# Performance work log

Hardware: AMD Instinct MI355X
Metric: run time of the kernel (lower is better)

Reference implementation:

```python
import jax, jax.numpy as jnp
import numpy as np

N_NODES = 50000
N_EDGES = 800000
N_FEAT = 128
HIDDEN = 256
N_GRAPHS = 256
N_CLASSES = 10
BN_EPS = 1e-5


def setup_inputs() -> dict:
    key = jax.random.key(0)
    ks = jax.random.split(key, 12)
    s = 1.0 / np.sqrt(HIDDEN)
    inp = {
        "x": jax.random.normal(ks[0], (N_NODES, N_FEAT), dtype=jnp.float32),
        "edge_index": jax.random.randint(ks[1], (2, N_EDGES), 0, N_NODES, dtype=jnp.int64),
        "batch": jnp.sort(jax.random.randint(ks[2], (N_NODES,), 0, N_GRAPHS, dtype=jnp.int64)),
        "conv1_w0": jax.random.normal(ks[3], (N_FEAT, HIDDEN), dtype=jnp.float32) / np.sqrt(N_FEAT),
        "conv1_b0": jnp.zeros((HIDDEN,), jnp.float32),
        "conv1_w1": jax.random.normal(ks[4], (HIDDEN, HIDDEN), dtype=jnp.float32) * s,
        "conv1_b1": jnp.zeros((HIDDEN,), jnp.float32),
        "conv1_bn_gamma": jnp.ones((HIDDEN,), jnp.float32),
        "conv1_bn_beta": jnp.zeros((HIDDEN,), jnp.float32),
        "conv1_bn_mean": jnp.zeros((HIDDEN,), jnp.float32),
        "conv1_bn_var": jnp.ones((HIDDEN,), jnp.float32),
        "convs_w0": jax.random.normal(ks[5], (3, HIDDEN, HIDDEN), dtype=jnp.float32) * s,
        "convs_b0": jnp.zeros((3, HIDDEN), jnp.float32),
        "convs_w1": jax.random.normal(ks[6], (3, HIDDEN, HIDDEN), dtype=jnp.float32) * s,
        "convs_b1": jnp.zeros((3, HIDDEN), jnp.float32),
        "convs_bn_gamma": jnp.ones((3, HIDDEN), jnp.float32),
        "convs_bn_beta": jnp.zeros((3, HIDDEN), jnp.float32),
        "convs_bn_mean": jnp.zeros((3, HIDDEN), jnp.float32),
        "convs_bn_var": jnp.ones((3, HIDDEN), jnp.float32),
        "eps": jnp.zeros((4,), jnp.float32),
        "lin1_w": jax.random.normal(ks[7], (HIDDEN, HIDDEN), dtype=jnp.float32) * s,
        "lin1_b": jnp.zeros((HIDDEN,), jnp.float32),
        "lin2_w": jax.random.normal(ks[8], (HIDDEN, N_CLASSES), dtype=jnp.float32) * s,
        "lin2_b": jnp.zeros((N_CLASSES,), jnp.float32),
    }
    return inp


def _gin_conv(x, src, dst, eps, w0, b0, w1, b1, g, be, m, v):
    # message = x[src]; aggregate = scatter_add at dst; update = MLP((1+eps)*x + aggr)
    aggr = jax.ops.segment_sum(x[src], dst, num_segments=N_NODES)
    h = (1.0 + eps) * x + aggr
    h = jax.nn.relu(h @ w0 + b0)
    h = jax.nn.relu(h @ w1 + b1)
    return (h - m) * jax.lax.rsqrt(v + BN_EPS) * g + be  # eval-mode BatchNorm1d


def reference(x, edge_index, batch,
              conv1_w0, conv1_b0, conv1_w1, conv1_b1,
              conv1_bn_gamma, conv1_bn_beta, conv1_bn_mean, conv1_bn_var,
              convs_w0, convs_b0, convs_w1, convs_b1,
              convs_bn_gamma, convs_bn_beta, convs_bn_mean, convs_bn_var,
              eps, lin1_w, lin1_b, lin2_w, lin2_b):
    src, dst = edge_index[0], edge_index[1]
    h = _gin_conv(x, src, dst, eps[0], conv1_w0, conv1_b0, conv1_w1, conv1_b1,
                  conv1_bn_gamma, conv1_bn_beta, conv1_bn_mean, conv1_bn_var)
    for i in range(convs_w0.shape[0]):
        h = _gin_conv(h, src, dst, eps[i + 1], convs_w0[i], convs_b0[i],
                      convs_w1[i], convs_b1[i], convs_bn_gamma[i], convs_bn_beta[i],
                      convs_bn_mean[i], convs_bn_var[i])
    # global_mean_pool over graph ids
    sums = jax.ops.segment_sum(h, batch, num_segments=N_GRAPHS)
    cnts = jax.ops.segment_sum(jnp.ones((N_NODES,), h.dtype), batch, num_segments=N_GRAPHS)
    pooled = sums / jnp.maximum(cnts, 1.0)[:, None]
    h = jax.nn.relu(pooled @ lin1_w + lin1_b)  # dropout is identity at inference
    logits = h @ lin2_w + lin2_b
    return jax.nn.log_softmax(logits, axis=-1)
```

## Files before the change

### kernel.cpp

```cpp
#include <hip/hip_runtime.h>
#include <hip/hip_bf16.h>

#define N_NODES 50000
#define N_EDGES 800000
#define N_FEAT 128
#define HIDDEN 256
#define N_GRAPHS 256
#define N_CLASSES 10
#define SCAN_NB ((N_NODES + 255) / 256)

typedef __hip_bfloat16 bf16_t;
typedef short bf16x8 __attribute__((ext_vector_type(8)));
typedef float f32x4 __attribute__((ext_vector_type(4)));

__device__ inline float bfb2f(short s) {
    unsigned u = ((unsigned)(unsigned short)s) << 16;
    float f; __builtin_memcpy(&f, &u, 4); return f;
}
__device__ inline short f2bfb(float f) {
    bf16_t b = __float2bfloat16(f);
    short s; __builtin_memcpy(&s, &b, 2); return s;
}


__global__ void count_deg_kernel(const int* __restrict__ ei, unsigned* __restrict__ deg) {
    int e = blockIdx.x * blockDim.x + threadIdx.x;
    if (e < N_EDGES) atomicAdd(&deg[ei[N_EDGES + e]], 1u);
}

__global__ __launch_bounds__(256) void scan_a_kernel(const unsigned* __restrict__ deg,
                                                     unsigned* __restrict__ rowptr,
                                                     unsigned* __restrict__ blocksum) {
    __shared__ unsigned tmp[256];
    int t = threadIdx.x;
    int g = blockIdx.x * 256 + t;
    unsigned v = (g < N_NODES) ? deg[g] : 0u;
    tmp[t] = v;
    __syncthreads();
    #pragma unroll
    for (int off = 1; off < 256; off <<= 1) {
        unsigned add = (t >= off) ? tmp[t - off] : 0u;
        __syncthreads();
        tmp[t] += add;
        __syncthreads();
    }
    if (g < N_NODES) rowptr[g] = tmp[t] - v;
    if (t == 255) blocksum[blockIdx.x] = tmp[t];
}

__global__ __launch_bounds__(256) void scan_b_kernel(unsigned* __restrict__ blocksum) {
    __shared__ unsigned tmp[256];
    int t = threadIdx.x;
    unsigned v = (t < SCAN_NB) ? blocksum[t] : 0u;
    tmp[t] = v;
    __syncthreads();
    #pragma unroll
    for (int off = 1; off < 256; off <<= 1) {
        unsigned add = (t >= off) ? tmp[t - off] : 0u;
        __syncthreads();
        tmp[t] += add;
        __syncthreads();
    }
    if (t < SCAN_NB) blocksum[t] = tmp[t] - v;
}

__global__ __launch_bounds__(256) void scan_c_kernel(unsigned* __restrict__ rowptr,
                                                     const unsigned* __restrict__ blocksum,
                                                     unsigned* __restrict__ cursor) {
    int g = blockIdx.x * 256 + threadIdx.x;
    if (g < N_NODES) {
        unsigned r = rowptr[g] + blocksum[blockIdx.x];
        rowptr[g] = r;
        cursor[g] = r;
    }
    if (g == 0) rowptr[N_NODES] = N_EDGES;
}

__global__ void fill_adj_kernel(const int* __restrict__ ei, unsigned* __restrict__ cursor,
                                int* __restrict__ adj) {
    int e = blockIdx.x * blockDim.x + threadIdx.x;
    if (e < N_EDGES) {
        int src = ei[e];
        int dst = ei[N_EDGES + e];
        unsigned pos = atomicAdd(&cursor[dst], 1u);
        adj[pos] = src;
    }
}


__global__ __launch_bounds__(256) void convert_x_kernel(const float* __restrict__ x,
                                                        bf16_t* __restrict__ xb) {
    int i = blockIdx.x * 256 + threadIdx.x;
    if (i < N_NODES * N_FEAT / 4) {
        float4 v = reinterpret_cast<const float4*>(x)[i];
        short4 o;
        o.x = f2bfb(v.x); o.y = f2bfb(v.y); o.z = f2bfb(v.z); o.w = f2bfb(v.w);
        reinterpret_cast<short4*>(xb)[i] = o;
    }
}


__global__ __launch_bounds__(256) void prep_weights_kernel(
    const float* __restrict__ c1_w0, const float* __restrict__ c1_w1,
    const float* __restrict__ cs_w0, const float* __restrict__ cs_w1,
    bf16_t* __restrict__ wt)
{
    __shared__ float T[32][33];
    int z = blockIdx.z;
    const float* src; int K; size_t off;
    if (z == 0)      { src = c1_w0; K = N_FEAT;  off = 0; }
    else if (z == 1) { src = c1_w1; K = HIDDEN;  off = 32768; }
    else {
        int i = (z - 2) >> 1;
        src = (((z - 2) & 1) ? cs_w1 : cs_w0) + (size_t)i * HIDDEN * HIDDEN;
        K = HIDDEN;
        off = 32768 + (size_t)(z - 1) * 65536;
    }
    int k0 = blockIdx.x * 32, n0 = blockIdx.y * 32;
    if (k0 >= K) return;
    int t = threadIdx.x;
    int r = t >> 3, c4 = (t & 7) * 4;
    float4 v = *reinterpret_cast<const float4*>(src + (size_t)(k0 + r) * HIDDEN + n0 + c4);
    T[r][c4 + 0] = v.x; T[r][c4 + 1] = v.y; T[r][c4 + 2] = v.z; T[r][c4 + 3] = v.w;
    __syncthreads();
    int n = t >> 3, kc = (t & 7) * 4;
    short4 o;
    o.x = f2bfb(T[kc + 0][n]); o.y = f2bfb(T[kc + 1][n]);
    o.z = f2bfb(T[kc + 2][n]); o.w = f2bfb(T[kc + 3][n]);
    *reinterpret_cast<short4*>((short*)wt + off + (size_t)(n0 + n) * K + k0 + kc) = o;
}


__global__ __launch_bounds__(256) void aggregate1_kernel(
    const bf16_t* __restrict__ xb, const int* __restrict__ adj,
    const unsigned* __restrict__ rowptr, const float* __restrict__ eps_arr,
    bf16_t* __restrict__ out)
{
    int w = threadIdx.x >> 6, lane = threadIdx.x & 63;
    int n = blockIdx.x * 4 + w;
    if (n >= N_NODES) return;
    int q = lane >> 4, l4 = lane & 15;
    unsigned beg = rowptr[n], end = rowptr[n + 1];
    const short* xs = (const short*)xb;
    float acc[8] = {};
    unsigned e = beg;
    for (; e + 8 <= end; e += 8) {
        int s0 = adj[e + q];
        int s1 = adj[e + 4 + q];
        bf16x8 v0 = *reinterpret_cast<const bf16x8*>(xs + (unsigned)s0 * N_FEAT + l4 * 8);
        bf16x8 v1 = *reinterpret_cast<const bf16x8*>(xs + (unsigned)s1 * N_FEAT + l4 * 8);
        #pragma unroll
        for (int j = 0; j < 8; j++) acc[j] += bfb2f(v0[j]) + bfb2f(v1[j]);
    }
    for (; e + 4 <= end; e += 4) {
        int s0 = adj[e + q];
        bf16x8 v0 = *reinterpret_cast<const bf16x8*>(xs + (unsigned)s0 * N_FEAT + l4 * 8);
        #pragma unroll
        for (int j = 0; j < 8; j++) acc[j] += bfb2f(v0[j]);
    }
    int rem = (int)(end - e);
    if (q < rem) {
        bf16x8 v0 = *reinterpret_cast<const bf16x8*>(xs + (unsigned)adj[e + q] * N_FEAT + l4 * 8);
        #pragma unroll
        for (int j = 0; j < 8; j++) acc[j] += bfb2f(v0[j]);
    }
    if (q == 0) {
        bf16x8 sv = *reinterpret_cast<const bf16x8*>(xs + (unsigned)n * N_FEAT + l4 * 8);
        float ep = 1.f + eps_arr[0];
        #pragma unroll
        for (int j = 0; j < 8; j++) acc[j] += ep * bfb2f(sv[j]);
    }
    #pragma unroll
    for (int j = 0; j < 8; j++) {
        acc[j] += __shfl_xor(acc[j], 16);
        acc[j] += __shfl_xor(acc[j], 32);
    }
    if (lane < 16) {
        bf16x8 o;
        #pragma unroll
        for (int j = 0; j < 8; j++) o[j] = f2bfb(acc[j]);
        *reinterpret_cast<bf16x8*>((short*)out + (unsigned)n * N_FEAT + l4 * 8) = o;
    }
}


__global__ __launch_bounds__(256) void aggregate2_kernel(
    const bf16_t* __restrict__ x, const int* __restrict__ adj,
    const unsigned* __restrict__ rowptr, const float* __restrict__ eps_arr, int eps_idx,
    bf16_t* __restrict__ out)
{
    int w = threadIdx.x >> 6, lane = threadIdx.x & 63;
    int n = blockIdx.x * 4 + w;
    if (n >= N_NODES) return;
    int half = lane >> 5, l5 = lane & 31;
    unsigned beg = rowptr[n], end = rowptr[n + 1];
    const short* xs = (const short*)x;
    float acc[8] = {};
    unsigned e = beg;
    for (; e + 8 <= end; e += 8) {
        int s0 = adj[e + half];
        int s1 = adj[e + 2 + half];
        int s2 = adj[e + 4 + half];
        int s3 = adj[e + 6 + half];
        bf16x8 v0 = *reinterpret_cast<const bf16x8*>(xs + (unsigned)s0 * HIDDEN + l5 * 8);
        bf16x8 v1 = *reinterpret_cast<const bf16x8*>(xs + (unsigned)s1 * HIDDEN + l5 * 8);
        bf16x8 v2 = *reinterpret_cast<const bf16x8*>(xs + (unsigned)s2 * HIDDEN + l5 * 8);
        bf16x8 v3 = *reinterpret_cast<const bf16x8*>(xs + (unsigned)s3 * HIDDEN + l5 * 8);
        #pragma unroll
        for (int j = 0; j < 8; j++)
            acc[j] += (bfb2f(v0[j]) + bfb2f(v1[j])) + (bfb2f(v2[j]) + bfb2f(v3[j]));
    }
    for (; e + 2 <= end; e += 2) {
        int s0 = adj[e + half];
        bf16x8 v0 = *reinterpret_cast<const bf16x8*>(xs + (unsigned)s0 * HIDDEN + l5 * 8);
        #pragma unroll
        for (int j = 0; j < 8; j++) acc[j] += bfb2f(v0[j]);
    }
    if (e < end && half == 0) {
        bf16x8 v0 = *reinterpret_cast<const bf16x8*>(xs + (unsigned)adj[e] * HIDDEN + l5 * 8);
        #pragma unroll
        for (int j = 0; j < 8; j++) acc[j] += bfb2f(v0[j]);
    }
    if (half == 0) {
        bf16x8 sv = *reinterpret_cast<const bf16x8*>(xs + (unsigned)n * HIDDEN + l5 * 8);
        float ep = 1.f + eps_arr[eps_idx];
        #pragma unroll
        for (int j = 0; j < 8; j++) acc[j] += ep * bfb2f(sv[j]);
    }
    #pragma unroll
    for (int j = 0; j < 8; j++) acc[j] += __shfl_xor(acc[j], 32);
    if (half == 0) {
        bf16x8 o;
        #pragma unroll
        for (int j = 0; j < 8; j++) o[j] = f2bfb(acc[j]);
        *reinterpret_cast<bf16x8*>((short*)out + (unsigned)n * HIDDEN + l5 * 8) = o;
    }
}


#define GBM 128
#define GBN 128
#define GBK 64

__global__ __launch_bounds__(512) void gemm_bf16_kernel(
    const bf16_t* __restrict__ A, const bf16_t* __restrict__ Wt,
    const float* __restrict__ bias, bf16_t* __restrict__ C,
    int M, int K,
    const float* __restrict__ bn_g, const float* __restrict__ bn_b,
    const float* __restrict__ bn_m, const float* __restrict__ bn_v, int do_bn)
{
    __shared__ short lds[18432];
    short (*As)[72] = reinterpret_cast<short(*)[72]>(lds);
    short (*Bs)[72] = reinterpret_cast<short(*)[72]>(lds + 9216);
    short (*Cs)[136] = reinterpret_cast<short(*)[136]>(lds);

    int tid = threadIdx.x;
    int lane = tid & 63;
    int wave = tid >> 6;
    int wr = wave >> 2, wc = wave & 3;
    int row0 = blockIdx.x * GBM, col0 = blockIdx.y * GBN;

    int lrow = tid >> 3, lch = tid & 7;

    const short* Ab = (const short*)A;
    const short* Wb = (const short*)Wt;

    f32x4 acc[4][2] = {};

    for (int k0 = 0; k0 < K; k0 += GBK) {
        #pragma unroll
        for (int rr = 0; rr < 2; rr++) {
            int r = lrow + rr * 64;
            int arow = row0 + r;
            bf16x8 av = {};
            if (arow < M)
                av = *reinterpret_cast<const bf16x8*>(Ab + (size_t)arow * K + k0 + lch * 8);
            *reinterpret_cast<bf16x8*>(&As[r][lch * 8]) = av;
            bf16x8 bv = *reinterpret_cast<const bf16x8*>(Wb + (size_t)(col0 + r) * K + k0 + lch * 8);
            *reinterpret_cast<bf16x8*>(&Bs[r][lch * 8]) = bv;
        }
        __syncthreads();

        int fr = lane & 15, fk = (lane >> 4) * 8;
        #pragma unroll
        for (int ks = 0; ks < 2; ks++) {
            bf16x8 a[4], b[2];
            #pragma unroll
            for (int m = 0; m < 4; m++)
                a[m] = *reinterpret_cast<const bf16x8*>(&As[wr * 64 + m * 16 + fr][ks * 32 + fk]);
            #pragma unroll
            for (int n = 0; n < 2; n++)
                b[n] = *reinterpret_cast<const bf16x8*>(&Bs[wc * 32 + n * 16 + fr][ks * 32 + fk]);
            #pragma unroll
            for (int m = 0; m < 4; m++)
                #pragma unroll
                for (int n = 0; n < 2; n++)
                    acc[m][n] = __builtin_amdgcn_mfma_f32_16x16x32_bf16(a[m], b[n], acc[m][n], 0, 0, 0);
        }
        __syncthreads();
    }

    #pragma unroll
    for (int m = 0; m < 4; m++) {
        #pragma unroll
        for (int n = 0; n < 2; n++) {
            int rl = wr * 64 + m * 16 + (lane >> 4) * 4;
            int cl = wc * 32 + n * 16 + (lane & 15);
            int c = col0 + cl;
            float bi = bias[c];
            #pragma unroll
            for (int r = 0; r < 4; r++) {
                float v = acc[m][n][r] + bi;
                v = fmaxf(v, 0.f);
                if (do_bn) v = (v - bn_m[c]) * rsqrtf(bn_v[c] + 1e-5f) * bn_g[c] + bn_b[c];
                Cs[rl + r][cl] = f2bfb(v);
            }
        }
    }
    __syncthreads();
    int lr = tid >> 2, c16 = tid & 3;
    int r = row0 + lr;
    if (r < M) {
        short* Cb = (short*)C;
        #pragma unroll
        for (int cc = 0; cc < 4; cc++) {
            int ch = c16 + cc * 4;
            bf16x8 cv = *reinterpret_cast<const bf16x8*>(&Cs[lr][ch * 8]);
            *reinterpret_cast<bf16x8*>(Cb + (size_t)r * HIDDEN + col0 + ch * 8) = cv;
        }
    }
}


__global__ __launch_bounds__(256) void pool_kernel(const bf16_t* __restrict__ h,
                                                   const int* __restrict__ batch,
                                                   float* __restrict__ pooled) {
    __shared__ int sbs[2];
    __shared__ float red[4][HIDDEN];
    int g = blockIdx.x;
    if (threadIdx.x == 0) {
        int lo = 0, hi = N_NODES;
        while (lo < hi) { int mid = (lo + hi) >> 1; if (batch[mid] < g) lo = mid + 1; else hi = mid; }
        sbs[0] = lo;
        hi = N_NODES;
        while (lo < hi) { int mid = (lo + hi) >> 1; if (batch[mid] < g + 1) lo = mid + 1; else hi = mid; }
        sbs[1] = lo;
    }
    __syncthreads();
    int sbeg = sbs[0], send = sbs[1];
    int w = threadIdx.x >> 6, lane = threadIdx.x & 63;
    int half = lane >> 5, l5 = lane & 31;
    const short* hb = (const short*)h;
    float acc[8] = {};
    for (int n = sbeg + w * 2 + half; n < send; n += 8) {
        bf16x8 v = *reinterpret_cast<const bf16x8*>(hb + (size_t)n * HIDDEN + l5 * 8);
        #pragma unroll
        for (int j = 0; j < 8; j++) acc[j] += bfb2f(v[j]);
    }
    #pragma unroll
    for (int j = 0; j < 8; j++) acc[j] += __shfl_xor(acc[j], 32);
    if (half == 0) {
        #pragma unroll
        for (int j = 0; j < 8; j++) red[w][l5 * 8 + j] = acc[j];
    }
    __syncthreads();
    int t = threadIdx.x;
    float s = red[0][t] + red[1][t] + red[2][t] + red[3][t];
    float cnt = (float)(send - sbeg);
    pooled[g * HIDDEN + t] = s / fmaxf(cnt, 1.f);
}


__global__ void head_kernel(const float* __restrict__ pooled,
                            const float* __restrict__ w1, const float* __restrict__ b1,
                            const float* __restrict__ w2, const float* __restrict__ b2,
                            float* __restrict__ out) {
    int g = blockIdx.x, t = threadIdx.x;
    __shared__ float p[HIDDEN];
    __shared__ float h1[HIDDEN];
    __shared__ float lg[N_CLASSES];
    p[t] = pooled[g * HIDDEN + t];
    __syncthreads();
    float acc = b1[t];
    for (int k = 0; k < HIDDEN; k++) acc += p[k] * w1[k * HIDDEN + t];
    h1[t] = fmaxf(acc, 0.f);
    __syncthreads();
    if (t < N_CLASSES) {
        float a = b2[t];
        for (int k = 0; k < HIDDEN; k++) a += h1[k] * w2[k * N_CLASSES + t];
        lg[t] = a;
    }
    __syncthreads();
    if (t == 0) {
        float mx = lg[0];
        for (int j = 1; j < N_CLASSES; j++) mx = fmaxf(mx, lg[j]);
        float se = 0.f;
        for (int j = 0; j < N_CLASSES; j++) se += expf(lg[j] - mx);
        float lse = mx + logf(se);
        for (int j = 0; j < N_CLASSES; j++) out[g * N_CLASSES + j] = lg[j] - lse;
    }
}


extern "C" void kernel_launch(void* const* d_in, const int* in_sizes, int n_in,
                              void* d_out, int out_size, void* d_ws, size_t ws_size,
                              hipStream_t stream) {
    const float* x       = (const float*)d_in[0];
    const int*   ei      = (const int*)d_in[1];
    const int*   batch   = (const int*)d_in[2];
    const float* c1_w0   = (const float*)d_in[3];
    const float* c1_b0   = (const float*)d_in[4];
    const float* c1_w1   = (const float*)d_in[5];
    const float* c1_b1   = (const float*)d_in[6];
    const float* c1_g    = (const float*)d_in[7];
    const float* c1_be   = (const float*)d_in[8];
    const float* c1_m    = (const float*)d_in[9];
    const float* c1_v    = (const float*)d_in[10];
    const float* cs_w0   = (const float*)d_in[11];
    const float* cs_b0   = (const float*)d_in[12];
    const float* cs_w1   = (const float*)d_in[13];
    const float* cs_b1   = (const float*)d_in[14];
    const float* cs_g    = (const float*)d_in[15];
    const float* cs_be   = (const float*)d_in[16];
    const float* cs_m    = (const float*)d_in[17];
    const float* cs_v    = (const float*)d_in[18];
    const float* eps     = (const float*)d_in[19];
    const float* lin1_w  = (const float*)d_in[20];
    const float* lin1_b  = (const float*)d_in[21];
    const float* lin2_w  = (const float*)d_in[22];
    const float* lin2_b  = (const float*)d_in[23];

    char* ws = (char*)d_ws;
    size_t off = 0;
    auto alloc = [&](size_t bytes) -> void* {
        void* p = ws + off;
        off += (bytes + 255) & ~(size_t)255;
        return p;
    };

    unsigned* deg      = (unsigned*)alloc(N_NODES * 4);
    unsigned* rowptr   = (unsigned*)alloc((N_NODES + 1) * 4);
    unsigned* cursor   = (unsigned*)alloc(N_NODES * 4);
    unsigned* blocksum = (unsigned*)alloc(SCAN_NB * 4);
    int*      adj      = (int*)alloc(N_EDGES * 4);
    bf16_t*   Wt       = (bf16_t*)alloc((size_t)(32768 + 7 * 65536) * 2);
    bf16_t*   xb       = (bf16_t*)alloc((size_t)N_NODES * N_FEAT * 2);
    bf16_t*   B1       = (bf16_t*)alloc((size_t)N_NODES * HIDDEN * 2);
    bf16_t*   B2       = (bf16_t*)alloc((size_t)N_NODES * HIDDEN * 2);
    bf16_t*   B3       = (bf16_t*)alloc((size_t)N_NODES * HIDDEN * 2);
    float*    pooled   = (float*)alloc(N_GRAPHS * HIDDEN * 4);

    bf16_t* wt_10 = Wt;
    bf16_t* wt_11 = Wt + 32768;
    auto wt_c0 = [&](int i) { return Wt + 32768 + (size_t)(1 + 2 * i) * 65536; };
    auto wt_c1 = [&](int i) { return Wt + 32768 + (size_t)(2 + 2 * i) * 65536; };

    hipMemsetAsync(deg, 0, N_NODES * 4, stream);

    int eb = (N_EDGES + 255) / 256;
    count_deg_kernel<<<eb, 256, 0, stream>>>(ei, deg);
    scan_a_kernel<<<SCAN_NB, 256, 0, stream>>>(deg, rowptr, blocksum);
    scan_b_kernel<<<1, 256, 0, stream>>>(blocksum);
    scan_c_kernel<<<SCAN_NB, 256, 0, stream>>>(rowptr, blocksum, cursor);
    fill_adj_kernel<<<eb, 256, 0, stream>>>(ei, cursor, adj);

    convert_x_kernel<<<(N_NODES * N_FEAT / 4 + 255) / 256, 256, 0, stream>>>(x, xb);
    prep_weights_kernel<<<dim3(8, 8, 8), 256, 0, stream>>>(c1_w0, c1_w1, cs_w0, cs_w1, Wt);

    dim3 ggrid((N_NODES + GBM - 1) / GBM, HIDDEN / GBN);
    int ab = (N_NODES + 3) / 4;

    aggregate1_kernel<<<ab, 256, 0, stream>>>(xb, adj, rowptr, eps, B1);
    gemm_bf16_kernel<<<ggrid, 512, 0, stream>>>(B1, wt_10, c1_b0, B2, N_NODES, N_FEAT,
                                                nullptr, nullptr, nullptr, nullptr, 0);
    gemm_bf16_kernel<<<ggrid, 512, 0, stream>>>(B2, wt_11, c1_b1, B3, N_NODES, HIDDEN,
                                                c1_g, c1_be, c1_m, c1_v, 1);

    for (int i = 0; i < 3; i++) {
        aggregate2_kernel<<<ab, 256, 0, stream>>>(B3, adj, rowptr, eps, i + 1, B1);
        gemm_bf16_kernel<<<ggrid, 512, 0, stream>>>(B1, wt_c0(i), cs_b0 + i * HIDDEN, B2,
                                                    N_NODES, HIDDEN,
                                                    nullptr, nullptr, nullptr, nullptr, 0);
        gemm_bf16_kernel<<<ggrid, 512, 0, stream>>>(B2, wt_c1(i), cs_b1 + i * HIDDEN, B3,
                                                    N_NODES, HIDDEN,
                                                    cs_g + i * HIDDEN, cs_be + i * HIDDEN,
                                                    cs_m + i * HIDDEN, cs_v + i * HIDDEN, 1);
    }

    pool_kernel<<<N_GRAPHS, 256, 0, stream>>>(B3, batch, pooled);
    head_kernel<<<N_GRAPHS, HIDDEN, 0, stream>>>(pooled, lin1_w, lin1_b, lin2_w, lin2_b, (float*)d_out);
}
```

Measured before the change: 523.1 us.

## Build CSR adjacency with two-level bucket sort using shared-memory atomics

Replaces the global-atomic degree count, three-kernel scan and atomic fill with a coarse bucket histogram per edge block, a single-block scan, a bucketed scatter of packed (src,dst) pairs, and a per-bucket fine fill. Atomics move from global memory to LDS, reducing contention and the number of kernels. The single-block scan walks all edge blocks serially per bucket, which adds a latency-bound step, and the change needs an extra 8-byte-per-edge buffer.

Measured after the change: 514.6 us. Within noise of the previous version (-1.6%).

```diff
diff --git a/kernel.cpp b/kernel.cpp
--- a/kernel.cpp
+++ b/kernel.cpp
@@ -7,7 +7,10 @@
 #define HIDDEN 256
 #define N_GRAPHS 256
 #define N_CLASSES 10
-#define SCAN_NB ((N_NODES + 255) / 256)
+
+#define NBUCK ((N_NODES + 255) / 256)
+#define EPB 2048
+#define NBLK_S ((N_EDGES + EPB - 1) / EPB)
 
 typedef __hip_bfloat16 bf16_t;
 typedef short bf16x8 __attribute__((ext_vector_type(8)));
@@ -23,67 +26,106 @@
 }
 
 
-__global__ void count_deg_kernel(const int* __restrict__ ei, unsigned* __restrict__ deg) {
-    int e = blockIdx.x * blockDim.x + threadIdx.x;
-    if (e < N_EDGES) atomicAdd(&deg[ei[N_EDGES + e]], 1u);
-}
-
-__global__ __launch_bounds__(256) void scan_a_kernel(const unsigned* __restrict__ deg,
-                                                     unsigned* __restrict__ rowptr,
-                                                     unsigned* __restrict__ blocksum) {
+__global__ __launch_bounds__(256) void bucket_hist_kernel(const int* __restrict__ ei,
+                                                          unsigned* __restrict__ histG) {
+    __shared__ unsigned lh[NBUCK];
+    int t = threadIdx.x, j = blockIdx.x;
+    for (int i = t; i < NBUCK; i += 256) lh[i] = 0;
+    __syncthreads();
+    int base = j * EPB;
+    #pragma unroll
+    for (int it = 0; it < EPB / 256; it++) {
+        int e = base + it * 256 + t;
+        if (e < N_EDGES) atomicAdd(&lh[(unsigned)ei[N_EDGES + e] >> 8], 1u);
+    }
+    __syncthreads();
+    for (int i = t; i < NBUCK; i += 256) histG[(size_t)j * NBUCK + i] = lh[i];
+}
+
+__global__ __launch_bounds__(256) void bucket_scan_kernel(unsigned* __restrict__ histG,
+                                                          unsigned* __restrict__ bucketBase) {
     __shared__ unsigned tmp[256];
     int t = threadIdx.x;
-    int g = blockIdx.x * 256 + t;
-    unsigned v = (g < N_NODES) ? deg[g] : 0u;
+    unsigned run = 0;
+    if (t < NBUCK) {
+        for (int j = 0; j < NBLK_S; j++) {
+            unsigned v = histG[(size_t)j * NBUCK + t];
+            histG[(size_t)j * NBUCK + t] = run;
+            run += v;
+        }
+    }
+    unsigned v = (t < NBUCK) ? run : 0;
     tmp[t] = v;
     __syncthreads();
+    for (int off = 1; off < 256; off <<= 1) {
+        unsigned a = (t >= off) ? tmp[t - off] : 0u;
+        __syncthreads();
+        tmp[t] += a;
+        __syncthreads();
+    }
+    unsigned base = tmp[t] - v;
+    if (t < NBUCK) {
+        bucketBase[t] = base;
+        for (int j = 0; j < NBLK_S; j++) histG[(size_t)j * NBUCK + t] += base;
+    }
+    if (t == NBUCK - 1) bucketBase[NBUCK] = base + v;
+}
+
+__global__ __launch_bounds__(256) void bucket_scatter_kernel(const int* __restrict__ ei,
+                                                             const unsigned* __restrict__ histG,
+                                                             unsigned long long* __restrict__ ebuf) {
+    __shared__ unsigned lcur[NBUCK];
+    int t = threadIdx.x, j = blockIdx.x;
+    for (int i = t; i < NBUCK; i += 256) lcur[i] = histG[(size_t)j * NBUCK + i];
+    __syncthreads();
+    int base = j * EPB;
     #pragma unroll
+    for (int it = 0; it < EPB / 256; it++) {
+        int e = base + it * 256 + t;
+        if (e < N_EDGES) {
+            unsigned src = (unsigned)ei[e];
+            unsigned dst = (unsigned)ei[N_EDGES + e];
+            unsigned pos = atomicAdd(&lcur[dst >> 8], 1u);
+            ebuf[pos] = (unsigned long long)src | ((unsigned long long)dst << 32);
+        }
+    }
+}
+
+__global__ __launch_bounds__(256) void fine_fill_kernel(const unsigned long long* __restrict__ ebuf,
+                                                        const unsigned* __restrict__ bucketBase,
+                                                        unsigned* __restrict__ rowptr,
+                                                        int* __restrict__ adj) {
+    __shared__ unsigned ldeg[256], lcur[256], tmp[256];
+    int b = blockIdx.x, t = threadIdx.x;
+    unsigned sbase = bucketBase[b];
+    int scnt = (int)(bucketBase[b + 1] - sbase);
+    ldeg[t] = 0;
+    __syncthreads();
+    for (int k = t; k < scnt; k += 256) {
+        unsigned dst = (unsigned)(ebuf[sbase + k] >> 32);
+        atomicAdd(&ldeg[dst & 255], 1u);
+    }
+    __syncthreads();
+    unsigned v = ldeg[t];
+    tmp[t] = v;
+    __syncthreads();
     for (int off = 1; off < 256; off <<= 1) {
-        unsigned add = (t >= off) ? tmp[t - off] : 0u;
+        unsigned a = (t >= off) ? tmp[t - off] : 0u;
         __syncthreads();
-        tmp[t] += add;
+        tmp[t] += a;
         __syncthreads();
     }
-    if (g < N_NODES) rowptr[g] = tmp[t] - v;
-    if (t == 255) blocksum[blockIdx.x] = tmp[t];
-}
-
-__global__ __launch_bounds__(256) void scan_b_kernel(unsigned* __restrict__ blocksum) {
-    __shared__ unsigned tmp[256];
-    int t = threadIdx.x;
-    unsigned v = (t < SCAN_NB) ? blocksum[t] : 0u;
-    tmp[t] = v;
-    __syncthreads();
-    #pragma unroll
-    for (int off = 1; off < 256; off <<= 1) {
-        unsigned add = (t >= off) ? tmp[t - off] : 0u;
-        __syncthreads();
-        tmp[t] += add;
-        __syncthreads();
-    }
-    if (t < SCAN_NB) blocksum[t] = tmp[t] - v;
-}
-
-__global__ __launch_bounds__(256) void scan_c_kernel(unsigned* __restrict__ rowptr,
-                                                     const unsigned* __restrict__ blocksum,
-                                                     unsigned* __restrict__ cursor) {
-    int g = blockIdx.x * 256 + threadIdx.x;
-    if (g < N_NODES) {
-        unsigned r = rowptr[g] + blocksum[blockIdx.x];
-        rowptr[g] = r;
-        cursor[g] = r;
-    }
-    if (g == 0) rowptr[N_NODES] = N_EDGES;
-}
-
-__global__ void fill_adj_kernel(const int* __restrict__ ei, unsigned* __restrict__ cursor,
-                                int* __restrict__ adj) {
-    int e = blockIdx.x * blockDim.x + threadIdx.x;
-    if (e < N_EDGES) {
-        int src = ei[e];
-        int dst = ei[N_EDGES + e];
-        unsigned pos = atomicAdd(&cursor[dst], 1u);
-        adj[pos] = src;
+    unsigned exc = tmp[t] - v;
+    lcur[t] = exc;
+    int gnode = b * 256 + t;
+    if (gnode < N_NODES) rowptr[gnode] = sbase + exc;
+    if (b == NBUCK - 1 && t == 0) rowptr[N_NODES] = N_EDGES;
+    __syncthreads();
+    for (int k = t; k < scnt; k += 256) {
+        unsigned long long p = ebuf[sbase + k];
+        unsigned dst = (unsigned)(p >> 32);
+        unsigned pos = atomicAdd(&lcur[dst & 255], 1u);
+        adj[sbase + pos] = (int)(p & 0xffffffffu);
     }
 }
 
@@ -438,31 +480,27 @@
         return p;
     };
 
-    unsigned* deg      = (unsigned*)alloc(N_NODES * 4);
-    unsigned* rowptr   = (unsigned*)alloc((N_NODES + 1) * 4);
-    unsigned* cursor   = (unsigned*)alloc(N_NODES * 4);
-    unsigned* blocksum = (unsigned*)alloc(SCAN_NB * 4);
-    int*      adj      = (int*)alloc(N_EDGES * 4);
-    bf16_t*   Wt       = (bf16_t*)alloc((size_t)(32768 + 7 * 65536) * 2);
-    bf16_t*   xb       = (bf16_t*)alloc((size_t)N_NODES * N_FEAT * 2);
-    bf16_t*   B1       = (bf16_t*)alloc((size_t)N_NODES * HIDDEN * 2);
-    bf16_t*   B2       = (bf16_t*)alloc((size_t)N_NODES * HIDDEN * 2);
-    bf16_t*   B3       = (bf16_t*)alloc((size_t)N_NODES * HIDDEN * 2);
-    float*    pooled   = (float*)alloc(N_GRAPHS * HIDDEN * 4);
+    unsigned* histG      = (unsigned*)alloc((size_t)NBLK_S * NBUCK * 4);
+    unsigned* bucketBase = (unsigned*)alloc((NBUCK + 1) * 4);
+    unsigned long long* ebuf = (unsigned long long*)alloc((size_t)N_EDGES * 8);
+    unsigned* rowptr     = (unsigned*)alloc((N_NODES + 1) * 4);
+    int*      adj        = (int*)alloc(N_EDGES * 4);
+    bf16_t*   Wt         = (bf16_t*)alloc((size_t)(32768 + 7 * 65536) * 2);
+    bf16_t*   xb         = (bf16_t*)alloc((size_t)N_NODES * N_FEAT * 2);
+    bf16_t*   B1         = (bf16_t*)alloc((size_t)N_NODES * HIDDEN * 2);
+    bf16_t*   B2         = (bf16_t*)alloc((size_t)N_NODES * HIDDEN * 2);
+    bf16_t*   B3         = (bf16_t*)alloc((size_t)N_NODES * HIDDEN * 2);
+    float*    pooled     = (float*)alloc(N_GRAPHS * HIDDEN * 4);
 
     bf16_t* wt_10 = Wt;
     bf16_t* wt_11 = Wt + 32768;
     auto wt_c0 = [&](int i) { return Wt + 32768 + (size_t)(1 + 2 * i) * 65536; };
     auto wt_c1 = [&](int i) { return Wt + 32768 + (size_t)(2 + 2 * i) * 65536; };
 
-    hipMemsetAsync(deg, 0, N_NODES * 4, stream);
-
-    int eb = (N_EDGES + 255) / 256;
-    count_deg_kernel<<<eb, 256, 0, stream>>>(ei, deg);
-    scan_a_kernel<<<SCAN_NB, 256, 0, stream>>>(deg, rowptr, blocksum);
-    scan_b_kernel<<<1, 256, 0, stream>>>(blocksum);
-    scan_c_kernel<<<SCAN_NB, 256, 0, stream>>>(rowptr, blocksum, cursor);
-    fill_adj_kernel<<<eb, 256, 0, stream>>>(ei, cursor, adj);
+    bucket_hist_kernel<<<NBLK_S, 256, 0, stream>>>(ei, histG);
+    bucket_scan_kernel<<<1, 256, 0, stream>>>(histG, bucketBase);
+    bucket_scatter_kernel<<<NBLK_S, 256, 0, stream>>>(ei, histG, ebuf);
+    fine_fill_kernel<<<NBUCK, 256, 0, stream>>>(ebuf, bucketBase, rowptr, adj);
 
     convert_x_kernel<<<(N_NODES * N_FEAT / 4 + 255) / 256, 256, 0, stream>>>(x, xb);
     prep_weights_kernel<<<dim3(8, 8, 8), 256, 0, stream>>>(c1_w0, c1_w1, cs_w0, cs_w1, Wt);
```
